# Performance work log

Hardware: AMD Instinct MI355X
Metric: run time of the kernel (lower is better)

Reference implementation:

```python
import jax, jax.numpy as jnp
import numpy as np

B, Dx, Dz, Dy, H = 4096, 512, 512, 256, 2048
T0, T1 = 0.0, 1.0
N_STEPS = 64


def setup_inputs() -> dict:
    key = jax.random.key(0)
    ks = jax.random.split(key, 9)
    X = jax.random.normal(ks[0], (B, Dx), jnp.float32)
    # P sampled Uniform(0.01, 0.1) as in the torch module
    P = jax.random.uniform(ks[1], (Dz, Dx), jnp.float32, 0.01, 0.1)
    # A scaled so spectral radius ~1 -> exp(A*T) stays bounded over the integration
    A = jax.random.normal(ks[2], (Dz, Dz), jnp.float32) * (Dz ** -0.5)
    W1 = jax.random.normal(ks[3], (H, Dz), jnp.float32) * (Dz ** -0.5)
    b1 = jax.random.normal(ks[4], (H,), jnp.float32) * 0.01
    W2 = jax.random.normal(ks[5], (H, H), jnp.float32) * (H ** -0.5)
    b2 = jax.random.normal(ks[6], (H,), jnp.float32) * 0.01
    W3 = jax.random.normal(ks[7], (Dy, H), jnp.float32) * (H ** -0.5)
    b3 = jax.random.normal(ks[8], (Dy,), jnp.float32) * 0.01
    return dict(X=X, P=P, A=A, W1=W1, b1=b1, W2=W2, b2=b2, W3=W3, b3=b3,
                n_steps=N_STEPS)


def reference(X, P, A, W1, b1, W2, b2, W3, b3, n_steps):
    # Z0 = einsum('ji,bi->bj', P, X)  -> projection into latent ODE state
    z0 = X @ P.T  # [B, Dz]
    dt = jnp.float32((T1 - T0) / n_steps)

    def f(z):  # dz/dt = A z, batched: einsum('ji,bi->bj', A, z)
        return z @ A.T

    def rk4_step(z, _):
        k1 = f(z)
        k2 = f(z + 0.5 * dt * k1)
        k3 = f(z + 0.5 * dt * k2)
        k4 = f(z + dt * k3)
        return z + (dt / 6.0) * (k1 + 2.0 * k2 + 2.0 * k3 + k4), None

    zT, _ = jax.lax.scan(rk4_step, z0, None, length=n_steps)  # [B, Dz]

    # QnnMatrixODE MLP head (n_layers=3): Lin+ReLU, Lin+ReLU, Lin
    h = jax.nn.relu(zT @ W1.T + b1)
    h = jax.nn.relu(h @ W2.T + b2)
    y = h @ W3.T + b3  # [B, Dy]
    return y
```

## Files before the change

kernel.cpp:

```cpp
#include <hip/hip_runtime.h>

#define BDIM 4096
#define DX 512
#define DZ 512
#define DY 256
#define HD 2048
#define LDT 72

typedef __attribute__((ext_vector_type(8))) short bf16x8;
typedef __attribute__((ext_vector_type(4))) float f32x4;

__device__ inline unsigned short f2bf(float f) {
    unsigned u = __float_as_uint(f);
    unsigned r = 0x7FFFu + ((u >> 16) & 1u);
    return (unsigned short)((u + r) >> 16);
}
__device__ inline float bf2f(unsigned short h) {
    return __uint_as_float(((unsigned)h) << 16);
}

#define GLDS16(g, l)                                                            \
    __builtin_amdgcn_global_load_lds((const __attribute__((address_space(1))) void*)(g), \
                                     (__attribute__((address_space(3))) void*)(l), 16, 0, 0)

struct PrepJobs {
    const float* src[7];
    unsigned short* hi[7];
    unsigned short* lo[7];
    int n4[7];
};
__global__ __launch_bounds__(256) void prep_k(PrepJobs J) {
    const int j = blockIdx.y;
    if (j < 6) {
        const int i4 = blockIdx.x * 256 + threadIdx.x;
        if (i4 >= J.n4[j]) return;
        float4 v = ((const float4*)J.src[j])[i4];
        ushort4 h;
        h.x = f2bf(v.x); h.y = f2bf(v.y); h.z = f2bf(v.z); h.w = f2bf(v.w);
        ((ushort4*)J.hi[j])[i4] = h;
        if (J.lo[j]) {
            ushort4 l;
            l.x = f2bf(v.x - bf2f(h.x));
            l.y = f2bf(v.y - bf2f(h.y));
            l.z = f2bf(v.z - bf2f(h.z));
            l.w = f2bf(v.w - bf2f(h.w));
            ((ushort4*)J.lo[j])[i4] = l;
        }
    } else {
        if (blockIdx.x >= 256) return;
        __shared__ float t[32][33];
        const float* A = J.src[6];
        unsigned short* HT = J.hi[6];
        unsigned short* LT = J.lo[6];
        const int bx = (blockIdx.x & 15) * 32, by = (blockIdx.x >> 4) * 32;
        const int x = threadIdx.x & 31, y = threadIdx.x >> 5;
#pragma unroll
        for (int dy = 0; dy < 32; dy += 8)
            t[y + dy][x] = A[(size_t)(by + y + dy) * DZ + bx + x];
        __syncthreads();
#pragma unroll
        for (int dy = 0; dy < 32; dy += 8) {
            float v = t[x][y + dy];
            unsigned short h = f2bf(v);
            size_t o = (size_t)(bx + y + dy) * DZ + by + x;
            HT[o] = h;
            LT[o] = f2bf(v - bf2f(h));
        }
    }
}

struct G64In { const unsigned short *Ahi, *Alo, *Bhi, *Blo; const float* Dadd; };
struct G64Out { float* Cf32; unsigned short *Chi, *Clo, *CThi, *CTlo; };
struct E0Out {
    const float* Af32;
    const unsigned short *A2h, *A2l;
    unsigned short *B0Th, *B0Tl, *B1Th, *B1Tl, *B2Th, *B2Tl;
};

__device__ __forceinline__ void g64_kloop(G64In in, int row0, int col0, int K,
                                          f32x4 (&acc)[4], int sr, int sk, int mb, int nb,
                                          unsigned short* Ash, unsigned short* Asl,
                                          unsigned short* Bsh, unsigned short* Bsl) {
    const int niter = K >> 6;
    bf16x8 pa0, pa1, pl0, pl1, pb0, pb1, pq0, pq1;
    {
        const unsigned short* ar = in.Ahi + (size_t)(row0 + sr) * K + sk;
        const unsigned short* al = in.Alo + (size_t)(row0 + sr) * K + sk;
        const unsigned short* br = in.Bhi + (size_t)(col0 + sr) * K + sk;
        const unsigned short* bl = in.Blo + (size_t)(col0 + sr) * K + sk;
        pa0 = *(const bf16x8*)ar; pa1 = *(const bf16x8*)(ar + 8);
        pl0 = *(const bf16x8*)al; pl1 = *(const bf16x8*)(al + 8);
        pb0 = *(const bf16x8*)br; pb1 = *(const bf16x8*)(br + 8);
        pq0 = *(const bf16x8*)bl; pq1 = *(const bf16x8*)(bl + 8);
    }

    for (int it = 0; it < niter; ++it) {
        __syncthreads();
        *(bf16x8*)&Ash[sr * LDT + sk] = pa0; *(bf16x8*)&Ash[sr * LDT + sk + 8] = pa1;
        *(bf16x8*)&Asl[sr * LDT + sk] = pl0; *(bf16x8*)&Asl[sr * LDT + sk + 8] = pl1;
        *(bf16x8*)&Bsh[sr * LDT + sk] = pb0; *(bf16x8*)&Bsh[sr * LDT + sk + 8] = pb1;
        *(bf16x8*)&Bsl[sr * LDT + sk] = pq0; *(bf16x8*)&Bsl[sr * LDT + sk + 8] = pq1;
        __syncthreads();

        {
            const int kn = (it + 1 < niter) ? ((it + 1) << 6) : 0;
            const unsigned short* ar = in.Ahi + (size_t)(row0 + sr) * K + kn + sk;
            const unsigned short* al = in.Alo + (size_t)(row0 + sr) * K + kn + sk;
            const unsigned short* br = in.Bhi + (size_t)(col0 + sr) * K + kn + sk;
            const unsigned short* bl = in.Blo + (size_t)(col0 + sr) * K + kn + sk;
            pa0 = *(const bf16x8*)ar; pa1 = *(const bf16x8*)(ar + 8);
            pl0 = *(const bf16x8*)al; pl1 = *(const bf16x8*)(al + 8);
            pb0 = *(const bf16x8*)br; pb1 = *(const bf16x8*)(br + 8);
            pq0 = *(const bf16x8*)bl; pq1 = *(const bf16x8*)(bl + 8);
        }

#pragma unroll
        for (int kh = 0; kh < 2; ++kh) {
            const int kk = kh * 32 + (threadIdx.x >> 4 & 3) * 8;
            bf16x8 ah[2], alx[2], bh[2], blx[2];
#pragma unroll
            for (int t = 0; t < 2; ++t) {
                ah[t]  = *(const bf16x8*)&Ash[(mb + t * 16) * LDT + kk];
                alx[t] = *(const bf16x8*)&Asl[(mb + t * 16) * LDT + kk];
                bh[t]  = *(const bf16x8*)&Bsh[(nb + t * 16) * LDT + kk];
                blx[t] = *(const bf16x8*)&Bsl[(nb + t * 16) * LDT + kk];
            }
#pragma unroll
            for (int mt = 0; mt < 2; ++mt)
#pragma unroll
                for (int nt = 0; nt < 2; ++nt) {
                    acc[mt * 2 + nt] = __builtin_amdgcn_mfma_f32_16x16x32_bf16(
                        ah[mt], bh[nt], acc[mt * 2 + nt], 0, 0, 0);
                    acc[mt * 2 + nt] = __builtin_amdgcn_mfma_f32_16x16x32_bf16(
                        ah[mt], blx[nt], acc[mt * 2 + nt], 0, 0, 0);
                    acc[mt * 2 + nt] = __builtin_amdgcn_mfma_f32_16x16x32_bf16(
                        alx[mt], bh[nt], acc[mt * 2 + nt], 0, 0, 0);
                }
        }
    }
}

template <int EPI>
__device__ __forceinline__ void g64_core(int bx, int by, int M, int N, int K,
                                         G64In in, G64Out o, E0Out e,
                                         unsigned short* Ash, unsigned short* Asl,
                                         unsigned short* Bsh, unsigned short* Bsl) {
    const int tid = threadIdx.x;
    const int lane = tid & 63;
    const int wave = tid >> 6;
    const int wr = wave >> 1, wc = wave & 1;
    const int row0 = by * 64, col0 = bx * 64;
    const int sr = tid >> 2;
    const int sk = (tid & 3) * 16;
    const int mb = wr * 32 + (lane & 15);
    const int nb = wc * 32 + (lane & 15);

    f32x4 acc[4] = {};
    g64_kloop(in, row0, col0, K, acc, sr, sk, mb, nb, Ash, Asl, Bsh, Bsl);

#pragma unroll
    for (int mt = 0; mt < 2; ++mt) {
        const int grow = row0 + wr * 32 + mt * 16 + (lane >> 4) * 4;
#pragma unroll
        for (int nt = 0; nt < 2; ++nt) {
            const int gcol = col0 + wc * 32 + nt * 16 + (lane & 15);
            f32x4 a = acc[mt * 2 + nt];
            if (EPI == 1) {
                ushort4 h0, l0, h1v, l1v, h2v, l2v;
                unsigned short* H0 = &h0.x;  unsigned short* L0 = &l0.x;
                unsigned short* H1 = &h1v.x; unsigned short* L1 = &l1v.x;
                unsigned short* H2 = &h2v.x; unsigned short* L2 = &l2v.x;
#pragma unroll
                for (int i = 0; i < 4; ++i) {
                    const size_t idx = (size_t)(grow + i) * N + gcol;
                    const float di = (grow + i == gcol) ? 1.0f : 0.0f;
                    const float av = e.Af32[idx];
                    const float a2v = bf2f(e.A2h[idx]) + bf2f(e.A2l[idx]);
                    const float a3v = a[i];
                    float b0 = di + av + 0.5f * a2v + 1.6666667e-1f * a3v;
                    float b1 = 4.1666668e-2f * di + 8.3333333e-3f * av +
                               1.3888889e-3f * a2v + 1.9841270e-4f * a3v;
                    float b2 = 2.4801587e-5f * di + 2.7557319e-6f * av +
                               2.7557319e-7f * a2v + 2.5052108e-8f * a3v;
                    H0[i] = f2bf(b0); L0[i] = f2bf(b0 - bf2f(H0[i]));
                    H1[i] = f2bf(b1); L1[i] = f2bf(b1 - bf2f(H1[i]));
                    H2[i] = f2bf(b2); L2[i] = f2bf(b2 - bf2f(H2[i]));
                }
                const size_t to = (size_t)gcol * DZ + grow;
                *(ushort4*)&e.B0Th[to] = h0; *(ushort4*)&e.B0Tl[to] = l0;
                *(ushort4*)&e.B1Th[to] = h1v; *(ushort4*)&e.B1Tl[to] = l1v;
                *(ushort4*)&e.B2Th[to] = h2v; *(ushort4*)&e.B2Tl[to] = l2v;
            } else {
                if (in.Dadd) {
#pragma unroll
                    for (int i = 0; i < 4; ++i)
                        a[i] += in.Dadd[(size_t)(grow + i) * N + gcol];
                }
                unsigned short h4[4], l4[4];
#pragma unroll
                for (int i = 0; i < 4; ++i) {
                    h4[i] = f2bf(a[i]);
                    l4[i] = f2bf(a[i] - bf2f(h4[i]));
                }
                if (o.Cf32) {
#pragma unroll
                    for (int i = 0; i < 4; ++i) o.Cf32[(size_t)(grow + i) * N + gcol] = a[i];
                }
                if (o.Chi) {
#pragma unroll
                    for (int i = 0; i < 4; ++i) o.Chi[(size_t)(grow + i) * N + gcol] = h4[i];
                }
                if (o.Clo) {
#pragma unroll
                    for (int i = 0; i < 4; ++i) o.Clo[(size_t)(grow + i) * N + gcol] = l4[i];
                }
                if (o.CThi) {
                    ushort4 u = {h4[0], h4[1], h4[2], h4[3]};
                    *(ushort4*)&o.CThi[(size_t)gcol * M + grow] = u;
                }
                if (o.CTlo) {
                    ushort4 u = {l4[0], l4[1], l4[2], l4[3]};
                    *(ushort4*)&o.CTlo[(size_t)gcol * M + grow] = u;
                }
            }
        }
    }
}

template <int RELU, int BIAS, int OUT_BF16>
__device__ __forceinline__ void bigemm_core(int bxi, int byi, int M, int N, int K,
                                            const unsigned short* __restrict__ A,
                                            const unsigned short* __restrict__ B,
                                            void* __restrict__ C,
                                            const float* __restrict__ bias,
                                            unsigned short* As, unsigned short* Bs) {
    const int tid = threadIdx.x;
    const int lane = tid & 63;
    const int wave = tid >> 6;
    const int wr = wave >> 1, wc = wave & 1;
    const int row0 = byi * 64;
    const int col0 = bxi * 128;

    const int srow = lane >> 2;
    const int schunk = (lane & 3) * 8;

    f32x4 acc[2][4] = {};

    for (int k0 = 0; k0 < K; k0 += 32) {
        GLDS16(A + (size_t)(row0 + wave * 16 + srow) * K + k0 + schunk, &As[(wave * 16) * 32]);
        GLDS16(B + (size_t)(col0 + wave * 32 + srow) * K + k0 + schunk, &Bs[(wave * 32) * 32]);
        GLDS16(B + (size_t)(col0 + wave * 32 + 16 + srow) * K + k0 + schunk,
               &Bs[(wave * 32 + 16) * 32]);
        __syncthreads();

        const int kk = (lane >> 4) * 8;
        const int mbase = wr * 32 + (lane & 15);
        const int nbase = wc * 64 + (lane & 15);
        bf16x8 af[2], bf[4];
#pragma unroll
        for (int t = 0; t < 2; ++t) af[t] = *(const bf16x8*)&As[(mbase + t * 16) * 32 + kk];
#pragma unroll
        for (int t = 0; t < 4; ++t) bf[t] = *(const bf16x8*)&Bs[(nbase + t * 16) * 32 + kk];
#pragma unroll
        for (int mt = 0; mt < 2; ++mt)
#pragma unroll
            for (int nt = 0; nt < 4; ++nt)
                acc[mt][nt] = __builtin_amdgcn_mfma_f32_16x16x32_bf16(af[mt], bf[nt],
                                                                      acc[mt][nt], 0, 0, 0);
        __syncthreads();
    }

#pragma unroll
    for (int mt = 0; mt < 2; ++mt) {
        const int grow = row0 + wr * 32 + mt * 16 + (lane >> 4) * 4;
#pragma unroll
        for (int nt = 0; nt < 4; ++nt) {
            const int gcol = col0 + wc * 64 + nt * 16 + (lane & 15);
            const float bv = BIAS ? bias[gcol] : 0.0f;
#pragma unroll
            for (int i = 0; i < 4; ++i) {
                float v = acc[mt][nt][i] + bv;
                if (RELU) v = fmaxf(v, 0.0f);
                const size_t off = (size_t)(grow + i) * N + gcol;
                if (OUT_BF16)
                    ((unsigned short*)C)[off] = f2bf(v);
                else
                    ((float*)C)[off] = v;
            }
        }
    }
}

template <int RELU, int BIAS, int OUT_BF16>
__global__ __launch_bounds__(256) void gemm_bf16_v2(int M, int N, int K,
                                                    const unsigned short* __restrict__ A,
                                                    const unsigned short* __restrict__ B,
                                                    void* __restrict__ C,
                                                    const float* __restrict__ bias) {
    __shared__ unsigned short As[64 * 32];
    __shared__ unsigned short Bs[128 * 32];
    bigemm_core<RELU, BIAS, OUT_BF16>(blockIdx.x, blockIdx.y, M, N, K, A, B, C, bias, As, Bs);
}

__global__ __launch_bounds__(256) void combo_k(const unsigned short* Xb,
                                               const unsigned short* Pb,
                                               unsigned short* XPb,
                                               G64In ia, G64Out oa) {
    __shared__ __align__(16) unsigned short smem[4 * 64 * LDT];
    if (blockIdx.z == 0) {
        if (blockIdx.x >= DZ / 128) return;
        bigemm_core<0, 0, 1>(blockIdx.x, blockIdx.y, BDIM, DZ, DX, Xb, Pb, XPb, nullptr,
                             smem, smem + 64 * 32);
    } else {
        if (blockIdx.x >= 8 || blockIdx.y >= 8) return;
        E0Out e = {};
        g64_core<0>(blockIdx.x, blockIdx.y, DZ, DZ, DZ, ia, oa, e,
                    smem, smem + 64 * LDT, smem + 128 * LDT, smem + 192 * LDT);
    }
}

__global__ __launch_bounds__(256) void g64_dual_e0(G64In i0, E0Out e0o,
                                                   G64In i1, G64Out o1) {
    __shared__ __align__(16) unsigned short Ash[64 * LDT], Asl[64 * LDT];
    __shared__ __align__(16) unsigned short Bsh[64 * LDT], Bsl[64 * LDT];
    if (blockIdx.z == 0) {
        G64Out on = {};
        g64_core<1>(blockIdx.x, blockIdx.y, DZ, DZ, DZ, i0, on, e0o, Ash, Asl, Bsh, Bsl);
    } else {
        E0Out en = {};
        g64_core<0>(blockIdx.x, blockIdx.y, DZ, DZ, DZ, i1, o1, en, Ash, Asl, Bsh, Bsl);
    }
}

__global__ __launch_bounds__(256) void g64_quad(G64In i0, G64Out o0, G64In i1, G64Out o1,
                                                G64In i2, G64Out o2, G64In i3, G64Out o3) {
    __shared__ __align__(16) unsigned short Ash[64 * LDT], Asl[64 * LDT];
    __shared__ __align__(16) unsigned short Bsh[64 * LDT], Bsl[64 * LDT];
    const int z = blockIdx.z;
    if (z == 3 && blockIdx.y >= 8) return;
    G64In in = (z == 0) ? i0 : (z == 1) ? i1 : (z == 2) ? i2 : i3;
    G64Out o = (z == 0) ? o0 : (z == 1) ? o1 : (z == 2) ? o2 : o3;
    const int M = (z < 3) ? HD : DZ;
    E0Out e = {};
    g64_core<0>(blockIdx.x, blockIdx.y, M, DZ, DZ, in, o, e, Ash, Asl, Bsh, Bsl);
}

__global__ __launch_bounds__(256) void g64_c1(G64In s1, G64In s2,
                                              const float* __restrict__ U0,
                                              unsigned short* __restrict__ C1b) {
    __shared__ __align__(16) unsigned short Ash[64 * LDT], Asl[64 * LDT];
    __shared__ __align__(16) unsigned short Bsh[64 * LDT], Bsl[64 * LDT];
    const int tid = threadIdx.x;
    const int lane = tid & 63;
    const int wave = tid >> 6;
    const int wr = wave >> 1, wc = wave & 1;
    const int row0 = blockIdx.y * 64, col0 = blockIdx.x * 64;
    const int sr = tid >> 2, sk = (tid & 3) * 16;
    const int mb = wr * 32 + (lane & 15);
    const int nb = wc * 32 + (lane & 15);

    f32x4 acc[4] = {};
    g64_kloop(s1, row0, col0, DZ, acc, sr, sk, mb, nb, Ash, Asl, Bsh, Bsl);
    g64_kloop(s2, row0, col0, DZ, acc, sr, sk, mb, nb, Ash, Asl, Bsh, Bsl);

#pragma unroll
    for (int mt = 0; mt < 2; ++mt) {
        const int grow = row0 + wr * 32 + mt * 16 + (lane >> 4) * 4;
#pragma unroll
        for (int nt = 0; nt < 2; ++nt) {
            const int gcol = col0 + wc * 32 + nt * 16 + (lane & 15);
#pragma unroll
            for (int i = 0; i < 4; ++i) {
                const size_t idx = (size_t)(grow + i) * DZ + gcol;
                C1b[idx] = f2bf(acc[mt * 2 + nt][i] + U0[idx]);
            }
        }
    }
}

__global__ __launch_bounds__(256) void gemm64nt_y(int M, int N, int K,
                                                  const unsigned short* __restrict__ A,
                                                  const unsigned short* __restrict__ B,
                                                  float* __restrict__ C,
                                                  const float* __restrict__ bias) {
    __shared__ __align__(16) unsigned short As[64 * LDT];
    __shared__ __align__(16) unsigned short Bs[64 * LDT];
    const int tid = threadIdx.x;
    const int lane = tid & 63;
    const int wave = tid >> 6;
    const int wr = wave >> 1, wc = wave & 1;
    const int row0 = blockIdx.y * 64;
    const int col0 = blockIdx.x * 64;
    const int sr = tid >> 2, sk = (tid & 3) * 16;

    const int niter = K >> 6;
    bf16x8 pa0, pa1, pb0, pb1;
    {
        const unsigned short* ar = A + (size_t)(row0 + sr) * K + sk;
        const unsigned short* br = B + (size_t)(col0 + sr) * K + sk;
        pa0 = *(const bf16x8*)ar; pa1 = *(const bf16x8*)(ar + 8);
        pb0 = *(const bf16x8*)br; pb1 = *(const bf16x8*)(br + 8);
    }

    f32x4 acc[4] = {};
    const int mb = wr * 32 + (lane & 15);
    const int nb = wc * 32 + (lane & 15);

    for (int it = 0; it < niter; ++it) {
        __syncthreads();
        *(bf16x8*)&As[sr * LDT + sk] = pa0; *(bf16x8*)&As[sr * LDT + sk + 8] = pa1;
        *(bf16x8*)&Bs[sr * LDT + sk] = pb0; *(bf16x8*)&Bs[sr * LDT + sk + 8] = pb1;
        __syncthreads();

        {
            const int kn = (it + 1 < niter) ? ((it + 1) << 6) : 0;
            const unsigned short* ar = A + (size_t)(row0 + sr) * K + kn + sk;
            const unsigned short* br = B + (size_t)(col0 + sr) * K + kn + sk;
            pa0 = *(const bf16x8*)ar; pa1 = *(const bf16x8*)(ar + 8);
            pb0 = *(const bf16x8*)br; pb1 = *(const bf16x8*)(br + 8);
        }

#pragma unroll
        for (int kh = 0; kh < 2; ++kh) {
            const int kk = kh * 32 + (lane >> 4) * 8;
            bf16x8 af[2], bf[2];
#pragma unroll
            for (int t = 0; t < 2; ++t) {
                af[t] = *(const bf16x8*)&As[(mb + t * 16) * LDT + kk];
                bf[t] = *(const bf16x8*)&Bs[(nb + t * 16) * LDT + kk];
            }
#pragma unroll
            for (int mt = 0; mt < 2; ++mt)
#pragma unroll
                for (int nt = 0; nt < 2; ++nt)
                    acc[mt * 2 + nt] = __builtin_amdgcn_mfma_f32_16x16x32_bf16(
                        af[mt], bf[nt], acc[mt * 2 + nt], 0, 0, 0);
        }
    }

#pragma unroll
    for (int mt = 0; mt < 2; ++mt) {
        const int grow = row0 + wr * 32 + mt * 16 + (lane >> 4) * 4;
#pragma unroll
        for (int nt = 0; nt < 2; ++nt) {
            const int gcol = col0 + wc * 32 + nt * 16 + (lane & 15);
            const float bv = bias ? bias[gcol] : 0.0f;
#pragma unroll
            for (int i = 0; i < 4; ++i)
                C[(size_t)(grow + i) * N + gcol] = acc[mt * 2 + nt][i] + bv;
        }
    }
}

extern "C" void kernel_launch(void* const* d_in, const int* in_sizes, int n_in,
                              void* d_out, int out_size, void* d_ws, size_t ws_size,
                              hipStream_t stream) {
    const float* X  = (const float*)d_in[0];
    const float* P  = (const float*)d_in[1];
    const float* Am = (const float*)d_in[2];
    const float* W1 = (const float*)d_in[3];
    const float* b1 = (const float*)d_in[4];
    const float* W2 = (const float*)d_in[5];
    const float* b2 = (const float*)d_in[6];
    const float* W3 = (const float*)d_in[7];
    const float* b3 = (const float*)d_in[8];
    float* out = (float*)d_out;

    const size_t S = (size_t)DZ * DZ;
    const size_t SW = (size_t)HD * DZ;

    char* p = (char*)d_ws;
    auto alloc_h = [&](size_t n) { unsigned short* r = (unsigned short*)p; p += ((n * 2 + 15) & ~15ull); return r; };
    unsigned short* Xb   = alloc_h((size_t)BDIM * DX);
    unsigned short* W2b  = alloc_h((size_t)HD * HD);
    unsigned short* W3b  = alloc_h((size_t)DY * HD);
    unsigned short* W1h  = alloc_h(SW);
    unsigned short* W1l  = alloc_h(SW);
    unsigned short* Pb   = alloc_h(S);
    unsigned short* Ah   = alloc_h(S);
    unsigned short* Al   = alloc_h(S);
    unsigned short* ATh  = alloc_h(S);
    unsigned short* ATl  = alloc_h(S);
    unsigned short* A2h  = alloc_h(S);
    unsigned short* A2l  = alloc_h(S);
    unsigned short* A2Th = alloc_h(S);
    unsigned short* A2Tl = alloc_h(S);
    unsigned short* A4h  = alloc_h(S);
    unsigned short* A4l  = alloc_h(S);
    unsigned short* A4Th = alloc_h(S);
    unsigned short* A4Tl = alloc_h(S);
    unsigned short* A8Th = alloc_h(S);
    unsigned short* A8Tl = alloc_h(S);
    unsigned short* B0Th = alloc_h(S);
    unsigned short* B0Tl = alloc_h(S);
    unsigned short* B1Th = alloc_h(S);
    unsigned short* B1Tl = alloc_h(S);
    unsigned short* B2Th = alloc_h(S);
    unsigned short* B2Tl = alloc_h(S);
    unsigned short* U1h  = alloc_h(SW);
    unsigned short* U1l  = alloc_h(SW);
    unsigned short* U2h  = alloc_h(SW);
    unsigned short* U2l  = alloc_h(SW);
    unsigned short* C1b  = alloc_h(SW);
    unsigned short* XPb  = alloc_h((size_t)BDIM * DZ);
    unsigned short* h1b  = alloc_h((size_t)BDIM * HD);
    unsigned short* h2b  = alloc_h((size_t)BDIM * HD);
    float* U0f = (float*)Ah;

    PrepJobs J;
    J.src[0] = X;  J.hi[0] = Xb;  J.lo[0] = nullptr; J.n4[0] = BDIM * DX / 4;
    J.src[1] = W2; J.hi[1] = W2b; J.lo[1] = nullptr; J.n4[1] = HD * HD / 4;
    J.src[2] = W3; J.hi[2] = W3b; J.lo[2] = nullptr; J.n4[2] = DY * HD / 4;
    J.src[3] = W1; J.hi[3] = W1h; J.lo[3] = W1l;     J.n4[3] = (int)(SW / 4);
    J.src[4] = Am; J.hi[4] = Ah;  J.lo[4] = Al;      J.n4[4] = (int)(S / 4);
    J.src[5] = P;  J.hi[5] = Pb;  J.lo[5] = nullptr; J.n4[5] = (int)(S / 4);
    J.src[6] = Am; J.hi[6] = ATh; J.lo[6] = ATl;     J.n4[6] = 256;
    prep_k<<<dim3(HD * HD / 4 / 256, 7), 256, 0, stream>>>(J);

    {
        G64In ia{Ah, Al, ATh, ATl, nullptr};
        G64Out oa{nullptr, A2h, A2l, A2Th, A2Tl};
        combo_k<<<dim3(8, BDIM / 64, 2), 256, 0, stream>>>(Xb, Pb, XPb, ia, oa);
    }
    {
        G64In i0{A2h, A2l, ATh, ATl, nullptr};
        E0Out e0o{Am, A2h, A2l, B0Th, B0Tl, B1Th, B1Tl, B2Th, B2Tl};
        G64In i1{A2h, A2l, A2Th, A2Tl, nullptr};
        G64Out o1{nullptr, A4h, A4l, A4Th, A4Tl};
        g64_dual_e0<<<dim3(DZ / 64, DZ / 64, 2), 256, 0, stream>>>(i0, e0o, i1, o1);
    }
    {
        G64In i0{W1h, W1l, B0Th, B0Tl, nullptr};
        G64Out o0{U0f, nullptr, nullptr, nullptr, nullptr};
        G64In i1{W1h, W1l, B1Th, B1Tl, nullptr};
        G64Out o1{nullptr, U1h, U1l, nullptr, nullptr};
        G64In i2{W1h, W1l, B2Th, B2Tl, nullptr};
        G64Out o2{nullptr, U2h, U2l, nullptr, nullptr};
        G64In i3{A4h, A4l, A4Th, A4Tl, nullptr};
        G64Out o3{nullptr, nullptr, nullptr, A8Th, A8Tl};
        g64_quad<<<dim3(DZ / 64, HD / 64, 4), 256, 0, stream>>>(i0, o0, i1, o1, i2, o2, i3, o3);
    }
    {
        G64In s1{U1h, U1l, A4Th, A4Tl, nullptr};
        G64In s2{U2h, U2l, A8Th, A8Tl, nullptr};
        g64_c1<<<dim3(DZ / 64, HD / 64), 256, 0, stream>>>(s1, s2, U0f, C1b);
    }

    gemm_bf16_v2<1, 1, 1><<<dim3(HD / 128, BDIM / 64), 256, 0, stream>>>(
        BDIM, HD, DZ, XPb, C1b, h1b, b1);
    gemm_bf16_v2<1, 1, 1><<<dim3(HD / 128, BDIM / 64), 256, 0, stream>>>(
        BDIM, HD, HD, h1b, W2b, h2b, b2);
    gemm64nt_y<<<dim3(DY / 64, BDIM / 64), 256, 0, stream>>>(
        BDIM, DY, HD, h2b, W3b, out, b3);
}
```

Measured before the change: 258.6 us.

## Use 128x128 register-prefetched MFMA tile for MLP hidden-layer GEMMs

Replaces the 64x128-tile GEMM used for the two hidden MLP layers with a new 128x128-tile kernel. Each wave computes a 64x64 sub-tile with 16 MFMA accumulators, and the next K=64 slab is prefetched into registers while the current one is consumed from padded LDS. The larger tile halves the number of blocks and increases operand reuse per global load, at the cost of more registers and fewer blocks to fill the GPU.

```diff
diff --git a/kernel.cpp b/kernel.cpp
--- a/kernel.cpp
+++ b/kernel.cpp
@@ -292,14 +292,95 @@
 }
 
 template <int RELU, int BIAS, int OUT_BF16>
-__global__ __launch_bounds__(256) void gemm_bf16_v2(int M, int N, int K,
+__global__ __launch_bounds__(256) void gemm_bf16_v3(int M, int N, int K,
                                                     const unsigned short* __restrict__ A,
                                                     const unsigned short* __restrict__ B,
                                                     void* __restrict__ C,
                                                     const float* __restrict__ bias) {
-    __shared__ unsigned short As[64 * 32];
-    __shared__ unsigned short Bs[128 * 32];
-    bigemm_core<RELU, BIAS, OUT_BF16>(blockIdx.x, blockIdx.y, M, N, K, A, B, C, bias, As, Bs);
+    __shared__ __align__(16) unsigned short As[128 * LDT];
+    __shared__ __align__(16) unsigned short Bs[128 * LDT];
+    const int tid = threadIdx.x;
+    const int lane = tid & 63;
+    const int wave = tid >> 6;
+    const int wr = wave >> 1, wc = wave & 1;
+    const int row0 = blockIdx.y * 128;
+    const int col0 = blockIdx.x * 128;
+    const int sr = tid >> 1;
+    const int sk = (tid & 1) * 32;
+
+    const int niter = K >> 6;
+    bf16x8 pa[4], pb[4];
+    {
+        const unsigned short* ar = A + (size_t)(row0 + sr) * K + sk;
+        const unsigned short* br = B + (size_t)(col0 + sr) * K + sk;
+#pragma unroll
+        for (int i = 0; i < 4; ++i) {
+            pa[i] = *(const bf16x8*)(ar + 8 * i);
+            pb[i] = *(const bf16x8*)(br + 8 * i);
+        }
+    }
+
+    f32x4 acc[4][4] = {};
+    const int mb = wr * 64 + (lane & 15);
+    const int nb = wc * 64 + (lane & 15);
+
+    for (int it = 0; it < niter; ++it) {
+        __syncthreads();
+#pragma unroll
+        for (int i = 0; i < 4; ++i) {
+            *(bf16x8*)&As[sr * LDT + sk + 8 * i] = pa[i];
+            *(bf16x8*)&Bs[sr * LDT + sk + 8 * i] = pb[i];
+        }
+        __syncthreads();
+
+        {
+            const int kn = (it + 1 < niter) ? ((it + 1) << 6) : 0;
+            const unsigned short* ar = A + (size_t)(row0 + sr) * K + kn + sk;
+            const unsigned short* br = B + (size_t)(col0 + sr) * K + kn + sk;
+#pragma unroll
+            for (int i = 0; i < 4; ++i) {
+                pa[i] = *(const bf16x8*)(ar + 8 * i);
+                pb[i] = *(const bf16x8*)(br + 8 * i);
+            }
+        }
+
+#pragma unroll
+        for (int kh = 0; kh < 2; ++kh) {
+            const int kk = kh * 32 + (lane >> 4) * 8;
+            bf16x8 af[4], bf[4];
+#pragma unroll
+            for (int t = 0; t < 4; ++t) {
+                af[t] = *(const bf16x8*)&As[(mb + t * 16) * LDT + kk];
+                bf[t] = *(const bf16x8*)&Bs[(nb + t * 16) * LDT + kk];
+            }
+#pragma unroll
+            for (int mt = 0; mt < 4; ++mt)
+#pragma unroll
+                for (int nt = 0; nt < 4; ++nt)
+                    acc[mt][nt] = __builtin_amdgcn_mfma_f32_16x16x32_bf16(
+                        af[mt], bf[nt], acc[mt][nt], 0, 0, 0);
+        }
+    }
+
+#pragma unroll
+    for (int mt = 0; mt < 4; ++mt) {
+        const int grow = row0 + wr * 64 + mt * 16 + (lane >> 4) * 4;
+#pragma unroll
+        for (int nt = 0; nt < 4; ++nt) {
+            const int gcol = col0 + wc * 64 + nt * 16 + (lane & 15);
+            const float bv = BIAS ? bias[gcol] : 0.0f;
+#pragma unroll
+            for (int i = 0; i < 4; ++i) {
+                float v = acc[mt][nt][i] + bv;
+                if (RELU) v = fmaxf(v, 0.0f);
+                const size_t off = (size_t)(grow + i) * N + gcol;
+                if (OUT_BF16)
+                    ((unsigned short*)C)[off] = f2bf(v);
+                else
+                    ((float*)C)[off] = v;
+            }
+        }
+    }
 }
 
 __global__ __launch_bounds__(256) void combo_k(const unsigned short* Xb,
@@ -546,9 +627,9 @@
         g64_c1<<<dim3(DZ / 64, HD / 64), 256, 0, stream>>>(s1, s2, U0f, C1b);
     }
 
-    gemm_bf16_v2<1, 1, 1><<<dim3(HD / 128, BDIM / 64), 256, 0, stream>>>(
+    gemm_bf16_v3<1, 1, 1><<<dim3(HD / 128, BDIM / 128), 256, 0, stream>>>(
         BDIM, HD, DZ, XPb, C1b, h1b, b1);
-    gemm_bf16_v2<1, 1, 1><<<dim3(HD / 128, BDIM / 64), 256, 0, stream>>>(
+    gemm_bf16_v3<1, 1, 1><<<dim3(HD / 128, BDIM / 128), 256, 0, stream>>>(
         BDIM, HD, HD, h1b, W2b, h2b, b2);
     gemm64nt_y<<<dim3(DY / 64, BDIM / 64), 256, 0, stream>>>(
         BDIM, DY, HD, h2b, W3b, out, b3);
```

After: 251.3 us. 2.8% less time.
